# Performance work log

Hardware: AMD Instinct MI355X
Metric: run time of the kernel (lower is better)

Reference implementation:

```python
import jax, jax.numpy as jnp
import numpy as np

B, T, I, E, K, J = 4, 4096, 1024, 16, 512, 1024


def setup_inputs() -> dict:
    key = jax.random.key(0)
    k1, k2, k3 = jax.random.split(key, 3)
    X = jax.random.normal(k1, (B, T, I), dtype=jnp.float32)
    ind = jax.random.randint(k2, (B, E, K), 0, T, dtype=jnp.int64)
    bound = 1.0 / np.sqrt(J)
    W = jax.random.uniform(k3, (E, I, J), dtype=jnp.float32, minval=-bound, maxval=bound)
    return {"X": X, "ind": ind, "W": W}


def reference(X, ind, W):
    Bs, Ts, Is = X.shape
    _, Es, Ks = ind.shape
    # gather tokens per expert: [B, E*K, I] -> [B, E, K, I]
    idx = ind.reshape(Bs, Es * Ks)
    Xg = jnp.take_along_axis(X, idx[:, :, None], axis=1).reshape(Bs, Es, Ks, Is)
    # per-expert GEMM
    Y = jnp.einsum('beki,eij->bekj', Xg, W)
    return Y
```

## Files before the change

### kernel.cpp

```cpp
#include <hip/hip_runtime.h>
#include <cstdint>
#include <cstddef>


typedef float    floatx4 __attribute__((ext_vector_type(4)));
typedef int      intx4   __attribute__((ext_vector_type(4)));
typedef _Float16 half8   __attribute__((ext_vector_type(8)));
typedef _Float16 half4v  __attribute__((ext_vector_type(4)));

constexpr int Bc = 4, Tc = 4096, Ic = 1024, Ec = 16, Kc = 512, Jc = 1024;
constexpr int BM = 128, BN = 128, BK = 64, NT = 256;
constexpr int AS = BK + 8;

__global__ void cvt_x_kernel(const float* __restrict__ X, _Float16* __restrict__ Xh, int n4) {
  int i = blockIdx.x * blockDim.x + threadIdx.x;
  int stride = gridDim.x * blockDim.x;
  for (; i < n4; i += stride) {
    floatx4 v = ((const floatx4*)X)[i];
    half4v h;
    h.x = (_Float16)v.x; h.y = (_Float16)v.y; h.z = (_Float16)v.z; h.w = (_Float16)v.w;
    ((half4v*)Xh)[i] = h;
  }
}

__global__ void cvt_w_kernel(const float* __restrict__ W, _Float16* __restrict__ WT) {
  __shared__ float tile[64][65];
  int bid = blockIdx.x;
  int e  = bid >> 8;
  int i0 = ((bid >> 4) & 15) * 64;
  int j0 = (bid & 15) * 64;
  int tid = threadIdx.x;
  int r  = tid >> 4;
  int c4 = tid & 15;
  const float* src = W + ((size_t)e << 20) + (size_t)i0 * Jc + j0;
#pragma unroll
  for (int s = 0; s < 4; s++) {
    int rr = r + s * 16;
    floatx4 v = *(const floatx4*)(src + (size_t)rr * Jc + c4 * 4);
    tile[rr][c4 * 4 + 0] = v.x; tile[rr][c4 * 4 + 1] = v.y;
    tile[rr][c4 * 4 + 2] = v.z; tile[rr][c4 * 4 + 3] = v.w;
  }
  __syncthreads();
  int jj = tid >> 2;
  int ig = tid & 3;
  half8 hv0, hv1;
#pragma unroll
  for (int q = 0; q < 8; q++) hv0[q] = (_Float16)tile[ig * 16 + q][jj];
#pragma unroll
  for (int q = 0; q < 8; q++) hv1[q] = (_Float16)tile[ig * 16 + 8 + q][jj];
  _Float16* dst = WT + ((size_t)e << 20) + (size_t)(j0 + jj) * Ic + i0 + ig * 16;
  ((half8*)dst)[0] = hv0;
  ((half8*)dst)[1] = hv1;
}

template <bool PRE>
__global__ __launch_bounds__(NT, 2) void gemm_kernel(
    const float* __restrict__ X, const int* __restrict__ ind32,
    const float* __restrict__ W,
    const _Float16* __restrict__ Xh, const _Float16* __restrict__ WT,
    float* __restrict__ Y) {
  __shared__ _Float16 As[BM * AS];
  __shared__ _Float16 Bs[BN * AS];
  __shared__ int rowid[BM];
  __shared__ int is64_s;

  const int tid = threadIdx.x;
  const int bid = blockIdx.x;
  constexpr int NTILE = Jc / BN;
  constexpr int MTILE = Kc / BM;
  const int tileid = bid % (NTILE * MTILE);
  const int be = bid / (NTILE * MTILE);
  const int mt = tileid / NTILE;
  const int nt = tileid % NTILE;
  const int b = be / Ec, e = be % Ec;
  const int k0 = mt * BM;
  const int j0 = nt * BN;

  if (tid == 0) {
    int orv = 0;
    for (int q = 1; q < 256; q += 2) orv |= ind32[q];
    is64_s = (orv == 0) ? 1 : 0;
  }
  __syncthreads();
  if (tid < BM) {
    int idx = be * Kc + k0 + tid;
    rowid[tid] = is64_s ? ind32[2 * idx] : ind32[idx];
  }
  __syncthreads();

  const int lane = tid & 63;
  const int wave = tid >> 6;
  const int wm = (wave >> 1) * 64;
  const int wn = (wave & 1) * 64;
  const int quad = lane >> 4;
  const int tr = lane & 15;

  floatx4 acc[4][4];
#pragma unroll
  for (int mi = 0; mi < 4; mi++)
#pragma unroll
    for (int ni = 0; ni < 4; ni++) acc[mi][ni] = {0.f, 0.f, 0.f, 0.f};

  for (int kk0 = 0; kk0 < Ic; kk0 += BK) {
    if constexpr (PRE) {
#pragma unroll
      for (int it = 0; it < 4; it++) {
        int c = tid + it * NT;
        int row = c >> 3, kc = c & 7;
        const _Float16* src = Xh + ((size_t)b * Tc + rowid[row]) * Ic + kk0 + kc * 8;
        *(intx4*)&As[row * AS + kc * 8] = *(const intx4*)src;
      }
#pragma unroll
      for (int it = 0; it < 4; it++) {
        int c = tid + it * NT;
        int row = c >> 3, kc = c & 7;
        const _Float16* src = WT + ((size_t)e * Jc + j0 + row) * Ic + kk0 + kc * 8;
        *(intx4*)&Bs[row * AS + kc * 8] = *(const intx4*)src;
      }
    } else {
#pragma unroll
      for (int it = 0; it < 4; it++) {
        int c = tid + it * NT;
        int row = c >> 3, kc = c & 7;
        const float* src = X + ((size_t)b * Tc + rowid[row]) * Ic + kk0 + kc * 8;
        floatx4 v0 = *(const floatx4*)src;
        floatx4 v1 = *(const floatx4*)(src + 4);
        half8 h;
        h[0] = (_Float16)v0.x; h[1] = (_Float16)v0.y; h[2] = (_Float16)v0.z; h[3] = (_Float16)v0.w;
        h[4] = (_Float16)v1.x; h[5] = (_Float16)v1.y; h[6] = (_Float16)v1.z; h[7] = (_Float16)v1.w;
        *(half8*)&As[row * AS + kc * 8] = h;
      }
      {
        int n = tid & 127;
        int kh = tid >> 7;
        const float* src = W + ((size_t)e * Ic + kk0 + kh * 32) * Jc + j0 + n;
        _Float16 hv[32];
#pragma unroll
        for (int q = 0; q < 32; q++) hv[q] = (_Float16)src[(size_t)q * Jc];
#pragma unroll
        for (int g = 0; g < 4; g++) {
          half8 hh;
#pragma unroll
          for (int q = 0; q < 8; q++) hh[q] = hv[g * 8 + q];
          *(half8*)&Bs[n * AS + kh * 32 + g * 8] = hh;
        }
      }
    }
    __syncthreads();

#pragma unroll
    for (int ks = 0; ks < 2; ks++) {
      const int kk = ks * 32;
      half8 af[4], bf[4];
#pragma unroll
      for (int mi = 0; mi < 4; mi++)
        af[mi] = *(const half8*)&As[(wm + mi * 16 + tr) * AS + kk + quad * 8];
#pragma unroll
      for (int ni = 0; ni < 4; ni++)
        bf[ni] = *(const half8*)&Bs[(wn + ni * 16 + tr) * AS + kk + quad * 8];
#pragma unroll
      for (int mi = 0; mi < 4; mi++)
#pragma unroll
        for (int ni = 0; ni < 4; ni++)
          acc[mi][ni] = __builtin_amdgcn_mfma_f32_16x16x32_f16(af[mi], bf[ni], acc[mi][ni], 0, 0, 0);
    }
    __syncthreads();
  }

  float* Yb = Y + (size_t)be * Kc * Jc;
#pragma unroll
  for (int mi = 0; mi < 4; mi++) {
#pragma unroll
    for (int ni = 0; ni < 4; ni++) {
      const int col = j0 + wn + ni * 16 + tr;
#pragma unroll
      for (int r = 0; r < 4; r++) {
        const int row = k0 + wm + mi * 16 + quad * 4 + r;
        Yb[(size_t)row * Jc + col] = acc[mi][ni][r];
      }
    }
  }
}

extern "C" void kernel_launch(void* const* d_in, const int* in_sizes, int n_in,
                              void* d_out, int out_size, void* d_ws, size_t ws_size,
                              hipStream_t stream) {
  const float* X = (const float*)d_in[0];
  const int* ind = (const int*)d_in[1];
  const float* W = (const float*)d_in[2];
  float* Y = (float*)d_out;

  const size_t nx = (size_t)Bc * Tc * Ic;
  const size_t nw = (size_t)Ec * Ic * Jc;
  const size_t need = (nx + nw) * sizeof(_Float16);
  const int gemm_grid = Bc * Ec * (Kc / BM) * (Jc / BN);

  if (ws_size >= need) {
    _Float16* Xh = (_Float16*)d_ws;
    _Float16* WT = Xh + nx;
    cvt_x_kernel<<<4096, NT, 0, stream>>>(X, Xh, (int)(nx / 4));
    cvt_w_kernel<<<Ec * 256, NT, 0, stream>>>(W, WT);
    gemm_kernel<true><<<gemm_grid, NT, 0, stream>>>(X, ind, W, Xh, WT, Y);
  } else {
    gemm_kernel<false><<<gemm_grid, NT, 0, stream>>>(X, ind, W, nullptr, nullptr, Y);
  }
}
```

Measured before the change: 353.6 us.

## Load GEMM tiles with direct global-to-LDS async copies and XOR swizzle

Replaces the register-staged global loads into padded LDS tiles with global_load_lds 16-byte direct copies into unpadded tiles. An XOR swizzle on the column chunk avoids bank conflicts in the MFMA fragment reads. Launch bounds are raised to target higher occupancy. The fp32 fallback path without workspace is removed, so the code now assumes the workspace is large enough.

```diff
diff --git a/kernel.cpp b/kernel.cpp
--- a/kernel.cpp
+++ b/kernel.cpp
@@ -4,13 +4,17 @@
 
 
 typedef float    floatx4 __attribute__((ext_vector_type(4)));
-typedef int      intx4   __attribute__((ext_vector_type(4)));
 typedef _Float16 half8   __attribute__((ext_vector_type(8)));
 typedef _Float16 half4v  __attribute__((ext_vector_type(4)));
 
 constexpr int Bc = 4, Tc = 4096, Ic = 1024, Ec = 16, Kc = 512, Jc = 1024;
 constexpr int BM = 128, BN = 128, BK = 64, NT = 256;
-constexpr int AS = BK + 8;
+
+__device__ __forceinline__ void async16(const void* g, void* l) {
+  __builtin_amdgcn_global_load_lds(
+      (const __attribute__((address_space(1))) uint32_t*)g,
+      (__attribute__((address_space(3))) uint32_t*)l, 16, 0, 0);
+}
 
 __global__ void cvt_x_kernel(const float* __restrict__ X, _Float16* __restrict__ Xh, int n4) {
   int i = blockIdx.x * blockDim.x + threadIdx.x;
@@ -53,26 +57,22 @@
   ((half8*)dst)[1] = hv1;
 }
 
-template <bool PRE>
-__global__ __launch_bounds__(NT, 2) void gemm_kernel(
-    const float* __restrict__ X, const int* __restrict__ ind32,
-    const float* __restrict__ W,
+__global__ __launch_bounds__(NT, 4) void gemm_kernel(
+    const int* __restrict__ ind32,
     const _Float16* __restrict__ Xh, const _Float16* __restrict__ WT,
     float* __restrict__ Y) {
-  __shared__ _Float16 As[BM * AS];
-  __shared__ _Float16 Bs[BN * AS];
+  __shared__ alignas(16) _Float16 As[BM * BK];
+  __shared__ alignas(16) _Float16 Bs[BN * BK];
   __shared__ int rowid[BM];
   __shared__ int is64_s;
 
   const int tid = threadIdx.x;
   const int bid = blockIdx.x;
-  constexpr int NTILE = Jc / BN;
-  constexpr int MTILE = Kc / BM;
-  const int tileid = bid % (NTILE * MTILE);
-  const int be = bid / (NTILE * MTILE);
-  const int mt = tileid / NTILE;
-  const int nt = tileid % NTILE;
-  const int b = be / Ec, e = be % Ec;
+  const int tileid = bid & 31;
+  const int be = bid >> 5;
+  const int mt = tileid >> 3;
+  const int nt = tileid & 7;
+  const int b = be >> 4, e = be & 15;
   const int k0 = mt * BM;
   const int j0 = nt * BN;
 
@@ -94,6 +94,19 @@
   const int wn = (wave & 1) * 64;
   const int quad = lane >> 4;
   const int tr = lane & 15;
+  const int t7 = tr & 7;
+  const int lr = lane >> 3;
+  const int cst = lane & 7;
+  const int cdat = cst ^ lr;
+
+  const _Float16* aptr[4];
+  const _Float16* bptr[4];
+#pragma unroll
+  for (int q = 0; q < 4; q++) {
+    const int rowA = (wave * 4 + q) * 8 + lr;
+    aptr[q] = Xh + ((size_t)b * Tc + rowid[rowA]) * Ic + cdat * 8;
+    bptr[q] = WT + ((size_t)e * Jc + j0 + rowA) * Ic + cdat * 8;
+  }
 
   floatx4 acc[4][4];
 #pragma unroll
@@ -101,63 +114,25 @@
 #pragma unroll
     for (int ni = 0; ni < 4; ni++) acc[mi][ni] = {0.f, 0.f, 0.f, 0.f};
 
-  for (int kk0 = 0; kk0 < Ic; kk0 += BK) {
-    if constexpr (PRE) {
+  for (int kk = 0; kk < Ic; kk += BK) {
 #pragma unroll
-      for (int it = 0; it < 4; it++) {
-        int c = tid + it * NT;
-        int row = c >> 3, kc = c & 7;
-        const _Float16* src = Xh + ((size_t)b * Tc + rowid[row]) * Ic + kk0 + kc * 8;
-        *(intx4*)&As[row * AS + kc * 8] = *(const intx4*)src;
-      }
+    for (int q = 0; q < 4; q++)
+      async16(aptr[q] + kk, &As[(wave * 4 + q) * 512]);
 #pragma unroll
-      for (int it = 0; it < 4; it++) {
-        int c = tid + it * NT;
-        int row = c >> 3, kc = c & 7;
-        const _Float16* src = WT + ((size_t)e * Jc + j0 + row) * Ic + kk0 + kc * 8;
-        *(intx4*)&Bs[row * AS + kc * 8] = *(const intx4*)src;
-      }
-    } else {
-#pragma unroll
-      for (int it = 0; it < 4; it++) {
-        int c = tid + it * NT;
-        int row = c >> 3, kc = c & 7;
-        const float* src = X + ((size_t)b * Tc + rowid[row]) * Ic + kk0 + kc * 8;
-        floatx4 v0 = *(const floatx4*)src;
-        floatx4 v1 = *(const floatx4*)(src + 4);
-        half8 h;
-        h[0] = (_Float16)v0.x; h[1] = (_Float16)v0.y; h[2] = (_Float16)v0.z; h[3] = (_Float16)v0.w;
-        h[4] = (_Float16)v1.x; h[5] = (_Float16)v1.y; h[6] = (_Float16)v1.z; h[7] = (_Float16)v1.w;
-        *(half8*)&As[row * AS + kc * 8] = h;
-      }
-      {
-        int n = tid & 127;
-        int kh = tid >> 7;
-        const float* src = W + ((size_t)e * Ic + kk0 + kh * 32) * Jc + j0 + n;
-        _Float16 hv[32];
-#pragma unroll
-        for (int q = 0; q < 32; q++) hv[q] = (_Float16)src[(size_t)q * Jc];
-#pragma unroll
-        for (int g = 0; g < 4; g++) {
-          half8 hh;
-#pragma unroll
-          for (int q = 0; q < 8; q++) hh[q] = hv[g * 8 + q];
-          *(half8*)&Bs[n * AS + kh * 32 + g * 8] = hh;
-        }
-      }
-    }
+    for (int q = 0; q < 4; q++)
+      async16(bptr[q] + kk, &Bs[(wave * 4 + q) * 512]);
     __syncthreads();
 
 #pragma unroll
     for (int ks = 0; ks < 2; ks++) {
-      const int kk = ks * 32;
+      const int cofs = ((ks * 4 + quad) ^ t7) * 8;
       half8 af[4], bf[4];
 #pragma unroll
       for (int mi = 0; mi < 4; mi++)
-        af[mi] = *(const half8*)&As[(wm + mi * 16 + tr) * AS + kk + quad * 8];
+        af[mi] = *(const half8*)&As[(wm + mi * 16 + tr) * 64 + cofs];
 #pragma unroll
       for (int ni = 0; ni < 4; ni++)
-        bf[ni] = *(const half8*)&Bs[(wn + ni * 16 + tr) * AS + kk + quad * 8];
+        bf[ni] = *(const half8*)&Bs[(wn + ni * 16 + tr) * 64 + cofs];
 #pragma unroll
       for (int mi = 0; mi < 4; mi++)
 #pragma unroll
@@ -191,17 +166,11 @@
   float* Y = (float*)d_out;
 
   const size_t nx = (size_t)Bc * Tc * Ic;
-  const size_t nw = (size_t)Ec * Ic * Jc;
-  const size_t need = (nx + nw) * sizeof(_Float16);
+  _Float16* Xh = (_Float16*)d_ws;
+  _Float16* WT = Xh + nx;
+
+  cvt_x_kernel<<<4096, NT, 0, stream>>>(X, Xh, (int)(nx / 4));
+  cvt_w_kernel<<<Ec * 256, NT, 0, stream>>>(W, WT);
   const int gemm_grid = Bc * Ec * (Kc / BM) * (Jc / BN);
-
-  if (ws_size >= need) {
-    _Float16* Xh = (_Float16*)d_ws;
-    _Float16* WT = Xh + nx;
-    cvt_x_kernel<<<4096, NT, 0, stream>>>(X, Xh, (int)(nx / 4));
-    cvt_w_kernel<<<Ec * 256, NT, 0, stream>>>(W, WT);
-    gemm_kernel<true><<<gemm_grid, NT, 0, stream>>>(X, ind, W, Xh, WT, Y);
-  } else {
-    gemm_kernel<false><<<gemm_grid, NT, 0, stream>>>(X, ind, W, nullptr, nullptr, Y);
-  }
+  gemm_kernel<<<gemm_grid, NT, 0, stream>>>(ind, Xh, WT, Y);
 }
```

New measurement: 395.3 us. +11.8%, slower.
